# Optimization experiments

Hardware: AMD Instinct MI355X
Metric: run time of the kernel (lower is better)

## Reference

```python
import jax, jax.numpy as jnp
import numpy as np

POS_W = 1.0
ANG_W = 1.0
WID_W = 1.0
N = 1048560  # predictions (divisible by 17)
M = 8388480  # total GT grasps = sum(arange(N) % 17)


def setup_inputs() -> dict:
    key = jax.random.key(0)
    k1, k2 = jax.random.split(key)
    pred = jax.random.normal(k1, (N, 6), dtype=jnp.float32)
    all_targets = jax.random.normal(k2, (M, 6), dtype=jnp.float32)
    # ragged counts in [0, 16]; sum == M exactly
    target_counts = (jnp.arange(N, dtype=jnp.int64) % 17)
    return {"pred": pred, "all_targets": all_targets, "target_counts": target_counts}


def _smooth_l1(x):
    a = jnp.abs(x)
    return jnp.where(a < 1.0, 0.5 * x * x, a - 0.5)


def reference(pred, all_targets, target_counts):
    n = pred.shape[0]
    m = all_targets.shape[0]
    # segment id for each GT row (contiguous slices, order of target_counts)
    seg = jnp.repeat(jnp.arange(n), target_counts, total_repeat_length=m)  # (M,)
    p = pred[seg]  # (M,6) gathered predictions
    dp = p[:, :2] - all_targets[:, :2]
    da = p[:, 2:4] - all_targets[:, 2:4]
    dw = p[:, 4] - all_targets[:, 4]
    dist = (POS_W * jnp.sum(dp * dp, axis=-1)
            + ANG_W * jnp.sum(da * da, axis=-1)
            + WID_W * dw * dw)  # (M,)
    # ragged argmin per segment (first occurrence, like torch.argmin)
    min_d = jax.ops.segment_min(dist, seg, num_segments=n)  # (N,)
    row = jnp.arange(m)
    cand = jnp.where(dist == min_d[seg], row, m)
    arg = jax.ops.segment_min(cand, seg, num_segments=n)  # (N,) global row idx or m
    has = target_counts > 0
    gt = all_targets[jnp.where(has, jnp.clip(arg, 0, m - 1), 0)]  # (N,6)
    # fused per-prediction loss against the closest GT
    loss_pos = jnp.sum(_smooth_l1(pred[:, :2] - gt[:, :2]), axis=-1)
    loss_ang = jnp.sum(jnp.abs(pred[:, 2:4] - gt[:, 2:4]), axis=-1)
    loss_wid = _smooth_l1(pred[:, 4] - gt[:, 4])
    losses = jnp.where(has, POS_W * loss_pos + ANG_W * loss_ang + WID_W * loss_wid, 0.0)
    return jnp.mean(losses)  # reduction='mean'
```

## Files before the change

kernel.cpp:

```cpp
#include <hip/hip_runtime.h>
#include <math.h>

#define POS_W 1.0f
#define ANG_W 1.0f
#define WID_W 1.0f

__device__ __forceinline__ float smooth_l1(float x) {
    float a = fabsf(x);
    return a < 1.0f ? 0.5f * x * x : a - 0.5f;
}

__global__ void k_block_sums(const int* __restrict__ counts, int stride, int n,
                             int* __restrict__ blockSums) {
    int i = blockIdx.x * 256 + threadIdx.x;
    int c = (i < n) ? counts[(long long)i * stride] : 0;
    for (int off = 32; off > 0; off >>= 1) c += __shfl_down(c, off, 64);
    __shared__ int sdata[4];
    int lane = threadIdx.x & 63, wave = threadIdx.x >> 6;
    if (lane == 0) sdata[wave] = c;
    __syncthreads();
    if (threadIdx.x == 0)
        blockSums[blockIdx.x] = sdata[0] + sdata[1] + sdata[2] + sdata[3];
}

__global__ void k_scan_blocks(const int* __restrict__ blockSums, int nb,
                              int* __restrict__ blockOffs) {
    int t = threadIdx.x;
    int per = (nb + 255) / 256;
    int start = t * per;
    int end = min(start + per, nb);
    int sum = 0;
    for (int j = start; j < end; ++j) sum += blockSums[j];
    __shared__ int s[256];
    s[t] = sum;
    __syncthreads();
    for (int d = 1; d < 256; d <<= 1) {
        int v = (t >= d) ? s[t - d] : 0;
        __syncthreads();
        s[t] += v;
        __syncthreads();
    }
    int run = s[t] - sum;
    for (int j = start; j < end; ++j) {
        blockOffs[j] = run;
        run += blockSums[j];
    }
}

__global__ __launch_bounds__(256) void k_loss(
    const float* __restrict__ pred, const float* __restrict__ tgt,
    const int* __restrict__ counts, int stride, int n,
    const int* __restrict__ blockOffs, float* __restrict__ partials) {
    __shared__ float2 buf[4][2][768];
    __shared__ int wsum[4];

    int t = threadIdx.x;
    int lane = t & 63, wave = t >> 6;
    int i = blockIdx.x * 256 + t;
    int c = (i < n) ? counts[(long long)i * stride] : 0;

    int incl = c;
#pragma unroll
    for (int d = 1; d < 64; d <<= 1) {
        int v = __shfl_up(incl, d, 64);
        if (lane >= d) incl += v;
    }
    if (lane == 63) wsum[wave] = incl;
    __syncthreads();
    int w0 = wsum[0], w1 = wsum[1], w2 = wsum[2];
    int waveOff = (wave > 0 ? w0 : 0) + (wave > 1 ? w1 : 0) + (wave > 2 ? w2 : 0);
    int offW = incl - c;
    int totalW = wsum[wave];
    const float2* win = (const float2*)tgt +
                        (long long)(blockOffs[blockIdx.x] + waveOff) * 3;

    bool active = (i < n) && (c > 0);
    float p0 = 0, p1 = 0, p2 = 0, p3 = 0, p4 = 0;
    if (i < n) {
        const float2* p2p = (const float2*)(pred + (long long)i * 6);
        float2 a = p2p[0], b = p2p[1], w = p2p[2];
        p0 = a.x; p1 = a.y; p2 = b.x; p3 = b.y; p4 = w.x;
    }

    float best = INFINITY;
    float b0 = 0, b1 = 0, b2 = 0, b3 = 0, b4 = 0;

    if (totalW > 0) {
        int totalF2 = totalW * 3;
        float2 r[12];
        float2(*mybuf)[768] = buf[wave];
#pragma unroll
        for (int j = 0; j < 12; ++j)
            r[j] = win[min(lane + 64 * j, totalF2 - 1)];

        int nch = (totalW + 255) >> 8;
        for (int ck = 0; ck < nch; ++ck) {
            float2* bb = mybuf[ck & 1];
#pragma unroll
            for (int j = 0; j < 12; ++j) bb[lane + 64 * j] = r[j];
            if (ck + 1 < nch) {
                int kb = (ck + 1) * 768 + lane;
#pragma unroll
                for (int j = 0; j < 12; ++j)
                    r[j] = win[min(kb + 64 * j, totalF2 - 1)];
            }
            asm volatile("s_waitcnt lgkmcnt(0)" ::: "memory");
            __builtin_amdgcn_wave_barrier();
            int base = ck << 8;
            int lo = max(offW, base), hi = min(offW + c, base + 256);
            for (int rr = lo; rr < hi; ++rr) {
                int l3 = (rr - base) * 3;
                float2 ga = bb[l3], gb = bb[l3 + 1], gw = bb[l3 + 2];
                float d0 = p0 - ga.x, d1 = p1 - ga.y;
                float d2 = p2 - gb.x, d3 = p3 - gb.y;
                float d4 = p4 - gw.x;
                float dist = POS_W * (d0 * d0 + d1 * d1) +
                             ANG_W * (d2 * d2 + d3 * d3) + WID_W * d4 * d4;
                if (dist < best) {
                    best = dist;
                    b0 = ga.x; b1 = ga.y; b2 = gb.x; b3 = gb.y; b4 = gw.x;
                }
            }
            __builtin_amdgcn_wave_barrier();
        }
    }

    float loss = 0.0f;
    if (active) {
        loss = POS_W * (smooth_l1(p0 - b0) + smooth_l1(p1 - b1)) +
               ANG_W * (fabsf(p2 - b2) + fabsf(p3 - b3)) +
               WID_W * smooth_l1(p4 - b4);
    }
    for (int o = 32; o > 0; o >>= 1) loss += __shfl_down(loss, o, 64);
    if (lane == 0) partials[blockIdx.x * 4 + wave] = loss;
}

__global__ void k_reduce(const float* __restrict__ partials, int np,
                         float invN, float* __restrict__ out) {
    int t = threadIdx.x;
    float s = 0.0f;
    for (int j = t; j < np; j += 256) s += partials[j];
    for (int o = 32; o > 0; o >>= 1) s += __shfl_down(s, o, 64);
    __shared__ float fs[4];
    int lane = t & 63, wave = t >> 6;
    if (lane == 0) fs[wave] = s;
    __syncthreads();
    if (t == 0) out[0] = (fs[0] + fs[1] + fs[2] + fs[3]) * invN;
}

extern "C" void kernel_launch(void* const* d_in, const int* in_sizes, int n_in,
                              void* d_out, int out_size, void* d_ws,
                              size_t ws_size, hipStream_t stream) {
    const float* pred = (const float*)d_in[0];
    const float* tgt = (const float*)d_in[1];
    const int* counts = (const int*)d_in[2];
    int n = in_sizes[0] / 6;
    int stride = (in_sizes[2] == n) ? 1 : 2;
    int nb = (n + 255) / 256;

    int* blockSums = (int*)d_ws;
    int* blockOffs = blockSums + nb;
    float* partials = (float*)(blockOffs + nb);
    float* out = (float*)d_out;

    k_block_sums<<<nb, 256, 0, stream>>>(counts, stride, n, blockSums);
    k_scan_blocks<<<1, 256, 0, stream>>>(blockSums, nb, blockOffs);
    k_loss<<<nb, 256, 0, stream>>>(pred, tgt, counts, stride, n, blockOffs,
                                   partials);
    k_reduce<<<1, 256, 0, stream>>>(partials, 4 * nb, 1.0f / n, out);
}
```

Baseline: 321.5 us.

## Give each wave a 512-prediction span streamed through a persistent chunk ring

```diff
diff --git a/kernel.cpp b/kernel.cpp
--- a/kernel.cpp
+++ b/kernel.cpp
@@ -4,33 +4,39 @@
 #define POS_W 1.0f
 #define ANG_W 1.0f
 #define WID_W 1.0f
+#define PW 512
+#define NT 8
+#define CH 256
 
 __device__ __forceinline__ float smooth_l1(float x) {
     float a = fabsf(x);
     return a < 1.0f ? 0.5f * x * x : a - 0.5f;
 }
 
-__global__ void k_block_sums(const int* __restrict__ counts, int stride, int n,
-                             int* __restrict__ blockSums) {
-    int i = blockIdx.x * 256 + threadIdx.x;
-    int c = (i < n) ? counts[(long long)i * stride] : 0;
+__global__ void k_span_sums(const int* __restrict__ counts, int stride, int n,
+                            int* __restrict__ spanSums) {
+    int t = threadIdx.x;
+    long long i0 = (long long)blockIdx.x * PW + t;
+    long long i1 = i0 + 256;
+    int c = (i0 < n ? counts[i0 * stride] : 0) +
+            (i1 < n ? counts[i1 * stride] : 0);
     for (int off = 32; off > 0; off >>= 1) c += __shfl_down(c, off, 64);
     __shared__ int sdata[4];
-    int lane = threadIdx.x & 63, wave = threadIdx.x >> 6;
+    int lane = t & 63, wave = t >> 6;
     if (lane == 0) sdata[wave] = c;
     __syncthreads();
-    if (threadIdx.x == 0)
-        blockSums[blockIdx.x] = sdata[0] + sdata[1] + sdata[2] + sdata[3];
-}
-
-__global__ void k_scan_blocks(const int* __restrict__ blockSums, int nb,
-                              int* __restrict__ blockOffs) {
-    int t = threadIdx.x;
-    int per = (nb + 255) / 256;
+    if (t == 0)
+        spanSums[blockIdx.x] = sdata[0] + sdata[1] + sdata[2] + sdata[3];
+}
+
+__global__ void k_scan_spans(const int* __restrict__ spanSums, int nw,
+                             int* __restrict__ waveBase) {
+    int t = threadIdx.x;
+    int per = (nw + 255) / 256;
     int start = t * per;
-    int end = min(start + per, nb);
+    int end = min(start + per, nw);
     int sum = 0;
-    for (int j = start; j < end; ++j) sum += blockSums[j];
+    for (int j = start; j < end; ++j) sum += spanSums[j];
     __shared__ int s[256];
     s[t] = sum;
     __syncthreads();
@@ -42,97 +48,121 @@
     }
     int run = s[t] - sum;
     for (int j = start; j < end; ++j) {
-        blockOffs[j] = run;
-        run += blockSums[j];
+        waveBase[j] = run;
+        run += spanSums[j];
     }
+    if (end == nw) waveBase[nw] = run;
 }
 
 __global__ __launch_bounds__(256) void k_loss(
     const float* __restrict__ pred, const float* __restrict__ tgt,
-    const int* __restrict__ counts, int stride, int n,
-    const int* __restrict__ blockOffs, float* __restrict__ partials) {
-    __shared__ float2 buf[4][2][768];
-    __shared__ int wsum[4];
-
-    int t = threadIdx.x;
-    int lane = t & 63, wave = t >> 6;
-    int i = blockIdx.x * 256 + t;
-    int c = (i < n) ? counts[(long long)i * stride] : 0;
-
-    int incl = c;
-#pragma unroll
-    for (int d = 1; d < 64; d <<= 1) {
-        int v = __shfl_up(incl, d, 64);
-        if (lane >= d) incl += v;
-    }
-    if (lane == 63) wsum[wave] = incl;
-    __syncthreads();
-    int w0 = wsum[0], w1 = wsum[1], w2 = wsum[2];
-    int waveOff = (wave > 0 ? w0 : 0) + (wave > 1 ? w1 : 0) + (wave > 2 ? w2 : 0);
-    int offW = incl - c;
-    int totalW = wsum[wave];
-    const float2* win = (const float2*)tgt +
-                        (long long)(blockOffs[blockIdx.x] + waveOff) * 3;
-
-    bool active = (i < n) && (c > 0);
+    const int* __restrict__ counts, int stride, long long n,
+    const int* __restrict__ waveBase, int nw, float* __restrict__ partials) {
+    __shared__ float2 ring[4][2][CH * 3];
+
+    int t = threadIdx.x;
+    int lane = t & 63, wv = t >> 6;
+    int w = blockIdx.x * 4 + wv;
+    if (w >= nw) return;
+
+    long long predStart = (long long)w * PW;
+    int rowStart = waveBase[w];
+    int totalW = waveBase[w + 1] - rowStart;
+    int totalF2 = totalW * 3;
+    const float2* win = (const float2*)tgt + (long long)rowStart * 3;
+
+    int tIdx = -1, tEnd = 0;
+    int c = 0, cur = 0, segHi = 0;
     float p0 = 0, p1 = 0, p2 = 0, p3 = 0, p4 = 0;
-    if (i < n) {
-        const float2* p2p = (const float2*)(pred + (long long)i * 6);
-        float2 a = p2p[0], b = p2p[1], w = p2p[2];
-        p0 = a.x; p1 = a.y; p2 = b.x; p3 = b.y; p4 = w.x;
-    }
-
-    float best = INFINITY;
-    float b0 = 0, b1 = 0, b2 = 0, b3 = 0, b4 = 0;
+    float best = INFINITY, b0 = 0, b1 = 0, b2 = 0, b3 = 0, b4 = 0;
+    float lossAcc = 0.0f;
+
+    auto finalize = [&]() {
+        if (tIdx >= 0) {
+            long long ip = predStart + (long long)tIdx * 64 + lane;
+            if (ip < n && c > 0)
+                lossAcc += POS_W * (smooth_l1(p0 - b0) + smooth_l1(p1 - b1)) +
+                           ANG_W * (fabsf(p2 - b2) + fabsf(p3 - b3)) +
+                           WID_W * smooth_l1(p4 - b4);
+        }
+    };
+    auto advance = [&]() {
+        finalize();
+        ++tIdx;
+        long long ip = predStart + (long long)tIdx * 64 + lane;
+        c = (ip < n) ? counts[ip * stride] : 0;
+        int incl = c;
+#pragma unroll
+        for (int d = 1; d < 64; d <<= 1) {
+            int v = __shfl_up(incl, d, 64);
+            if (lane >= d) incl += v;
+        }
+        int tot = __shfl(incl, 63, 64);
+        int tBase = tEnd;
+        cur = tBase + incl - c;
+        segHi = cur + c;
+        tEnd = tBase + tot;
+        if (ip < n) {
+            const float2* pp = (const float2*)(pred + ip * 6);
+            float2 a = pp[0], b = pp[1], ww = pp[2];
+            p0 = a.x; p1 = a.y; p2 = b.x; p3 = b.y; p4 = ww.x;
+        }
+        best = INFINITY;
+        b0 = 0; b1 = 0; b2 = 0; b3 = 0; b4 = 0;
+    };
 
     if (totalW > 0) {
-        int totalF2 = totalW * 3;
         float2 r[12];
-        float2(*mybuf)[768] = buf[wave];
+        float2(*mybuf)[CH * 3] = ring[wv];
 #pragma unroll
         for (int j = 0; j < 12; ++j)
             r[j] = win[min(lane + 64 * j, totalF2 - 1)];
 
-        int nch = (totalW + 255) >> 8;
+        int nch = (totalW + CH - 1) / CH;
         for (int ck = 0; ck < nch; ++ck) {
             float2* bb = mybuf[ck & 1];
 #pragma unroll
             for (int j = 0; j < 12; ++j) bb[lane + 64 * j] = r[j];
             if (ck + 1 < nch) {
-                int kb = (ck + 1) * 768 + lane;
+                int kb = (ck + 1) * (CH * 3) + lane;
 #pragma unroll
                 for (int j = 0; j < 12; ++j)
                     r[j] = win[min(kb + 64 * j, totalF2 - 1)];
             }
             asm volatile("s_waitcnt lgkmcnt(0)" ::: "memory");
             __builtin_amdgcn_wave_barrier();
-            int base = ck << 8;
-            int lo = max(offW, base), hi = min(offW + c, base + 256);
-            for (int rr = lo; rr < hi; ++rr) {
-                int l3 = (rr - base) * 3;
-                float2 ga = bb[l3], gb = bb[l3 + 1], gw = bb[l3 + 2];
-                float d0 = p0 - ga.x, d1 = p1 - ga.y;
-                float d2 = p2 - gb.x, d3 = p3 - gb.y;
-                float d4 = p4 - gw.x;
-                float dist = POS_W * (d0 * d0 + d1 * d1) +
-                             ANG_W * (d2 * d2 + d3 * d3) + WID_W * d4 * d4;
-                if (dist < best) {
-                    best = dist;
-                    b0 = ga.x; b1 = ga.y; b2 = gb.x; b3 = gb.y; b4 = gw.x;
+
+            int r0 = ck * CH;
+            int cEnd = min(r0 + CH, totalW);
+            while (tIdx < NT - 1 && tEnd <= r0) advance();
+            for (;;) {
+                int hiRow = min(cEnd, tEnd);
+                int lo = max(cur, r0), hi = min(segHi, hiRow);
+                for (int rr = lo; rr < hi; ++rr) {
+                    int l3 = (rr - r0) * 3;
+                    float2 ga = bb[l3], gb = bb[l3 + 1], gw = bb[l3 + 2];
+                    float d0 = p0 - ga.x, d1 = p1 - ga.y;
+                    float d2 = p2 - gb.x, d3 = p3 - gb.y;
+                    float d4 = p4 - gw.x;
+                    float dist = POS_W * (d0 * d0 + d1 * d1) +
+                                 ANG_W * (d2 * d2 + d3 * d3) + WID_W * d4 * d4;
+                    if (dist < best) {
+                        best = dist;
+                        b0 = ga.x; b1 = ga.y; b2 = gb.x; b3 = gb.y; b4 = gw.x;
+                    }
                 }
+                if (hi > cur) cur = hi;
+                if (tEnd <= cEnd && tIdx < NT - 1) advance();
+                else break;
             }
             __builtin_amdgcn_wave_barrier();
         }
     }
-
-    float loss = 0.0f;
-    if (active) {
-        loss = POS_W * (smooth_l1(p0 - b0) + smooth_l1(p1 - b1)) +
-               ANG_W * (fabsf(p2 - b2) + fabsf(p3 - b3)) +
-               WID_W * smooth_l1(p4 - b4);
-    }
-    for (int o = 32; o > 0; o >>= 1) loss += __shfl_down(loss, o, 64);
-    if (lane == 0) partials[blockIdx.x * 4 + wave] = loss;
+    while (tIdx < NT - 1) advance();
+    finalize();
+
+    for (int o = 32; o > 0; o >>= 1) lossAcc += __shfl_down(lossAcc, o, 64);
+    if (lane == 0) partials[w] = lossAcc;
 }
 
 __global__ void k_reduce(const float* __restrict__ partials, int np,
@@ -156,16 +186,17 @@
     const int* counts = (const int*)d_in[2];
     int n = in_sizes[0] / 6;
     int stride = (in_sizes[2] == n) ? 1 : 2;
-    int nb = (n + 255) / 256;
-
-    int* blockSums = (int*)d_ws;
-    int* blockOffs = blockSums + nb;
-    float* partials = (float*)(blockOffs + nb);
+    int nw = (n + PW - 1) / PW;
+    int nbC = (nw + 3) / 4;
+
+    int* spanSums = (int*)d_ws;
+    int* waveBase = spanSums + nw;
+    float* partials = (float*)(waveBase + nw + 1);
     float* out = (float*)d_out;
 
-    k_block_sums<<<nb, 256, 0, stream>>>(counts, stride, n, blockSums);
-    k_scan_blocks<<<1, 256, 0, stream>>>(blockSums, nb, blockOffs);
-    k_loss<<<nb, 256, 0, stream>>>(pred, tgt, counts, stride, n, blockOffs,
-                                   partials);
-    k_reduce<<<1, 256, 0, stream>>>(partials, 4 * nb, 1.0f / n, out);
-}
+    k_span_sums<<<nw, 256, 0, stream>>>(counts, stride, n, spanSums);
+    k_scan_spans<<<1, 256, 0, stream>>>(spanSums, nw, waveBase);
+    k_loss<<<nbC, 256, 0, stream>>>(pred, tgt, counts, stride, (long long)n,
+                                    waveBase, nw, partials);
+    k_reduce<<<1, 256, 0, stream>>>(partials, nw, 1.0f / n, out);
+}
```

Measured after the change: 315.9 us. Within noise of the previous version (-1.8%).
